# Kernel optimization log

Measured on AMD Instinct MI355X. Metric: run time of the kernel, lower is better.

Reference implementation:

```python
import math
import jax, jax.numpy as jnp
import numpy as np

BASE_MASK_PROB = 0.15
ENTROPY_TARGET = 0.7
MIN_ACTIVE = 1
EPS = 1e-8
NEG_LOG_EPS = -math.log(1e-8)

B, H, S = 4, 16, 1024


def setup_inputs() -> dict:
    key = jax.random.key(0)
    k1, k2 = jax.random.split(key)
    weights = jax.random.uniform(k1, (B, H, S, S), dtype=jnp.float32)
    # uniform noise replaces torch.bernoulli: mask = (noise < keep_prob)
    noise = jax.random.uniform(k2, (B, H, S, S), dtype=jnp.float32)
    return {"weights": weights, "noise": noise}


def _xlogy(x, y):
    # matches torch.xlogy: 0 * log(0) == 0
    return jnp.where(x == 0.0, 0.0, x * jnp.log(jnp.where(x == 0.0, 1.0, y)))


def reference(weights, noise):
    seq_len = weights.shape[-1]
    dtype = weights.dtype

    # normalize rows; degenerate (near-zero) rows become uniform
    weight_sums = jnp.sum(weights, axis=-1, keepdims=True)
    needs_norm = weight_sums < EPS
    safe_sums = jnp.where(needs_norm, 1.0, weight_sums)
    w = jnp.where(needs_norm, 1.0 / seq_len, weights / safe_sums)

    # fused entropy, clamped to -log(eps)
    entropy = jnp.minimum(-jnp.sum(_xlogy(w, w), axis=-1), NEG_LOG_EPS)

    max_entropy = math.log(float(seq_len))
    norm_entropy = jnp.clip(entropy / max_entropy, 0.0, 1.0)
    adaptive_prob = BASE_MASK_PROB * (1.0 - norm_entropy)
    keep_prob = 1.0 - adaptive_prob[..., None]          # [B,H,S,1]

    # bernoulli(keep_prob) via supplied uniform noise
    mask = (noise < keep_prob).astype(dtype)            # [B,H,S,S]

    # min_active fallback: rows with too few kept entries keep their top-k
    k = min(MIN_ACTIVE, seq_len)
    active_count = jnp.sum(mask, axis=-1)
    needs_more = active_count < k                        # [B,H,S]
    _, top_idx = jax.lax.top_k(w, k)                     # [B,H,S,k]
    min_mask = jnp.sum(jax.nn.one_hot(top_idx, seq_len, dtype=dtype), axis=-2)
    mask = jnp.where(needs_more[..., None], min_mask, mask)

    # mask and renormalize; fall back to unmasked weights if row sum ~ 0
    masked = w * mask
    msum = jnp.sum(masked, axis=-1, keepdims=True)
    valid = msum > EPS
    final_weights = jnp.where(valid, masked / jnp.where(valid, msum, 1.0), w)

    mask_rate = 1.0 - jnp.mean(mask, axis=-1)
    target_entropy = jnp.full_like(entropy, max_entropy * ENTROPY_TARGET)
    return final_weights, entropy, mask_rate, target_entropy
```

## Files before the change

### kernel.cpp

```cpp
#include <hip/hip_runtime.h>
#include <math.h>

namespace {
constexpr int kS = 1024;
constexpr float kEps = 1e-8f;
constexpr float kNegLogEps = 18.420680743952367f;
constexpr float kMaxEntropy = 6.9314718055994531f;
constexpr float kInvMaxEntropy = 1.0f / 6.9314718055994531f;
constexpr float kTargetEntropy = 4.8520302639196169f;
constexpr float kBaseMaskProb = 0.15f;
typedef float f32x4 __attribute__((ext_vector_type(4)));
}

__global__ __launch_bounds__(256, 8)
void curriculum_kernel(const float* __restrict__ weights,
                       const float* __restrict__ noise,
                       float* __restrict__ out_w,
                       float* __restrict__ out_ent,
                       float* __restrict__ out_mrate,
                       float* __restrict__ out_tent,
                       int nrows)
{
    const int lane = threadIdx.x & 63;
    const int wid  = threadIdx.x >> 6;
    const int row  = blockIdx.x * 4 + wid;
    if (row >= nrows) return;

    const long long base = (long long)row * kS;
    const float4* __restrict__ wsrc = reinterpret_cast<const float4*>(weights + base);
    const float4* __restrict__ nsrc = reinterpret_cast<const float4*>(noise + base);

    float4 a0 = wsrc[lane];
    float4 a1 = wsrc[lane + 64];
    float4 a2 = wsrc[lane + 128];
    float4 a3 = wsrc[lane + 192];
    float4 b0 = nsrc[lane];
    float4 b1 = nsrc[lane + 64];
    float4 b2 = nsrc[lane + 128];
    float4 b3 = nsrc[lane + 192];

    float w[16];
    w[0]=a0.x;  w[1]=a0.y;  w[2]=a0.z;  w[3]=a0.w;
    w[4]=a1.x;  w[5]=a1.y;  w[6]=a1.z;  w[7]=a1.w;
    w[8]=a2.x;  w[9]=a2.y;  w[10]=a2.z; w[11]=a2.w;
    w[12]=a3.x; w[13]=a3.y; w[14]=a3.z; w[15]=a3.w;

    float s = 0.0f, p = 0.0f;
    #pragma unroll
    for (int i = 0; i < 16; ++i) {
        s += w[i];
        p += w[i] * __logf(fmaxf(w[i], 1e-37f));
    }

    #pragma unroll
    for (int o = 1; o < 64; o <<= 1) {
        s += __shfl_xor(s, o, 64);
        p += __shfl_xor(p, o, 64);
    }

    if (s < kEps) {
        #pragma unroll
        for (int i = 0; i < 16; ++i) w[i] = 1.0f / (float)kS;
        s = 1.0f;
        p = -kMaxEntropy;
    }

    const float inv_s   = 1.0f / s;
    const float entropy = fminf(__logf(s) - p * inv_s, kNegLogEps);
    const float nent    = fminf(fmaxf(entropy * kInvMaxEntropy, 0.0f), 1.0f);
    const float keep    = 1.0f - kBaseMaskProb * (1.0f - nent);

    float nz[16];
    nz[0]=b0.x;  nz[1]=b0.y;  nz[2]=b0.z;  nz[3]=b0.w;
    nz[4]=b1.x;  nz[5]=b1.y;  nz[6]=b1.z;  nz[7]=b1.w;
    nz[8]=b2.x;  nz[9]=b2.y;  nz[10]=b2.z; nz[11]=b2.w;
    nz[12]=b3.x; nz[13]=b3.y; nz[14]=b3.z; nz[15]=b3.w;

    unsigned mask = 0u;
    float msum = 0.0f, cntf = 0.0f;
    #pragma unroll
    for (int i = 0; i < 16; ++i) {
        if (nz[i] < keep) { mask |= (1u << i); msum += w[i]; cntf += 1.0f; }
    }

    const unsigned long long anyk = __ballot(mask != 0u);

    #pragma unroll
    for (int o = 1; o < 64; o <<= 1) {
        cntf += __shfl_xor(cntf, o, 64);
        msum += __shfl_xor(msum, o, 64);
    }

    if (anyk == 0ull) {
        float mxv = w[0];
        int   mxi = lane * 4;
        #pragma unroll
        for (int i = 1; i < 16; ++i) {
            const int idx = ((i >> 2) << 8) + lane * 4 + (i & 3);
            if (w[i] > mxv) { mxv = w[i]; mxi = idx; }
        }
        #pragma unroll
        for (int o = 1; o < 64; o <<= 1) {
            const float ov = __shfl_xor(mxv, o, 64);
            const int   oi = __shfl_xor(mxi, o, 64);
            if (ov > mxv || (ov == mxv && oi < mxi)) { mxv = ov; mxi = oi; }
        }
        mask = (((mxi >> 2) & 63) == lane) ? (1u << (((mxi >> 8) << 2) | (mxi & 3))) : 0u;
        msum = mxv;
        cntf = 1.0f;
    }

    const bool  valid = msum > kEps * s;
    const float scale = valid ? 1.0f / msum : inv_s;

    f32x4 f0, f1, f2, f3;
    #pragma unroll
    for (int i = 0; i < 16; ++i) {
        const float v = (valid && !((mask >> i) & 1u)) ? 0.0f : w[i] * scale;
        f32x4* dstv = (i < 4) ? &f0 : (i < 8) ? &f1 : (i < 12) ? &f2 : &f3;
        (*dstv)[i & 3] = v;
    }

    f32x4* __restrict__ dst = reinterpret_cast<f32x4*>(out_w + base);
    __builtin_nontemporal_store(f0, dst + lane);
    __builtin_nontemporal_store(f1, dst + lane + 64);
    __builtin_nontemporal_store(f2, dst + lane + 128);
    __builtin_nontemporal_store(f3, dst + lane + 192);

    if (lane == 0) out_ent[row]   = entropy;
    if (lane == 1) out_mrate[row] = 1.0f - cntf * (1.0f / (float)kS);
    if (lane == 2) out_tent[row]  = kTargetEntropy;
}

extern "C" void kernel_launch(void* const* d_in, const int* in_sizes, int n_in,
                              void* d_out, int out_size, void* d_ws, size_t ws_size,
                              hipStream_t stream)
{
    (void)n_in; (void)d_ws; (void)ws_size; (void)out_size;

    const float* weights = (const float*)d_in[0];
    const float* noise   = (const float*)d_in[1];
    const long long total = (long long)in_sizes[0];
    const int nrows = (int)(total / kS);

    float* out_w     = (float*)d_out;
    float* out_ent   = out_w + total;
    float* out_mrate = out_ent + nrows;
    float* out_tent  = out_mrate + nrows;

    const int blocks = (nrows + 3) / 4;
    hipLaunchKernelGGL(curriculum_kernel, dim3(blocks), dim3(256), 0, stream,
                       weights, noise, out_w, out_ent, out_mrate, out_tent, nrows);
}
```

Measured before the change: 143.4 us.

## Process multiple rows per wave with register prefetch of next row

Each wave now handles eight rows in a grid-stride loop, loading the next row's weights and noise into registers while the current row is reduced and written. The aim is to overlap global load latency with compute and to cut the number of launched blocks. It doubles register use and lowers occupancy (launch bounds 4 instead of 8). With fewer blocks the GPU may also be less evenly filled.

```diff
diff --git a/kernel.cpp b/kernel.cpp
--- a/kernel.cpp
+++ b/kernel.cpp
@@ -9,36 +9,19 @@
 constexpr float kInvMaxEntropy = 1.0f / 6.9314718055994531f;
 constexpr float kTargetEntropy = 4.8520302639196169f;
 constexpr float kBaseMaskProb = 0.15f;
+constexpr int kRowsPerWave = 8;
 typedef float f32x4 __attribute__((ext_vector_type(4)));
 }
 
-__global__ __launch_bounds__(256, 8)
-void curriculum_kernel(const float* __restrict__ weights,
-                       const float* __restrict__ noise,
-                       float* __restrict__ out_w,
-                       float* __restrict__ out_ent,
-                       float* __restrict__ out_mrate,
-                       float* __restrict__ out_tent,
-                       int nrows)
+__device__ __forceinline__ void process_row(
+    f32x4 a0, f32x4 a1, f32x4 a2, f32x4 a3,
+    f32x4 b0, f32x4 b1, f32x4 b2, f32x4 b3,
+    int row, int lane,
+    float* __restrict__ out_w,
+    float* __restrict__ out_ent,
+    float* __restrict__ out_mrate,
+    float* __restrict__ out_tent)
 {
-    const int lane = threadIdx.x & 63;
-    const int wid  = threadIdx.x >> 6;
-    const int row  = blockIdx.x * 4 + wid;
-    if (row >= nrows) return;
-
-    const long long base = (long long)row * kS;
-    const float4* __restrict__ wsrc = reinterpret_cast<const float4*>(weights + base);
-    const float4* __restrict__ nsrc = reinterpret_cast<const float4*>(noise + base);
-
-    float4 a0 = wsrc[lane];
-    float4 a1 = wsrc[lane + 64];
-    float4 a2 = wsrc[lane + 128];
-    float4 a3 = wsrc[lane + 192];
-    float4 b0 = nsrc[lane];
-    float4 b1 = nsrc[lane + 64];
-    float4 b2 = nsrc[lane + 128];
-    float4 b3 = nsrc[lane + 192];
-
     float w[16];
     w[0]=a0.x;  w[1]=a0.y;  w[2]=a0.z;  w[3]=a0.w;
     w[4]=a1.x;  w[5]=a1.y;  w[6]=a1.z;  w[7]=a1.w;
@@ -51,7 +34,6 @@
         s += w[i];
         p += w[i] * __logf(fmaxf(w[i], 1e-37f));
     }
-
     #pragma unroll
     for (int o = 1; o < 64; o <<= 1) {
         s += __shfl_xor(s, o, 64);
@@ -121,7 +103,7 @@
         (*dstv)[i & 3] = v;
     }
 
-    f32x4* __restrict__ dst = reinterpret_cast<f32x4*>(out_w + base);
+    f32x4* __restrict__ dst = reinterpret_cast<f32x4*>(out_w + ((long long)row << 10));
     __builtin_nontemporal_store(f0, dst + lane);
     __builtin_nontemporal_store(f1, dst + lane + 64);
     __builtin_nontemporal_store(f2, dst + lane + 128);
@@ -130,6 +112,46 @@
     if (lane == 0) out_ent[row]   = entropy;
     if (lane == 1) out_mrate[row] = 1.0f - cntf * (1.0f / (float)kS);
     if (lane == 2) out_tent[row]  = kTargetEntropy;
+}
+
+__global__ __launch_bounds__(256, 4)
+void curriculum_kernel(const float* __restrict__ weights,
+                       const float* __restrict__ noise,
+                       float* __restrict__ out_w,
+                       float* __restrict__ out_ent,
+                       float* __restrict__ out_mrate,
+                       float* __restrict__ out_tent,
+                       int nrows, int wstride)
+{
+    const int lane = threadIdx.x & 63;
+    int row = (blockIdx.x << 2) | (threadIdx.x >> 6);
+    if (row >= nrows) return;
+
+    const f32x4* __restrict__ ws = reinterpret_cast<const f32x4*>(weights + ((long long)row << 10));
+    const f32x4* __restrict__ ns = reinterpret_cast<const f32x4*>(noise   + ((long long)row << 10));
+    f32x4 a0 = ws[lane], a1 = ws[lane+64], a2 = ws[lane+128], a3 = ws[lane+192];
+    f32x4 b0 = ns[lane], b1 = ns[lane+64], b2 = ns[lane+128], b3 = ns[lane+192];
+
+    for (int k = 0; k < kRowsPerWave; ++k) {
+        const int nrow = row + wstride;
+        const bool pf = (k + 1 < kRowsPerWave) && (nrow < nrows);
+
+        f32x4 na0, na1, na2, na3, nb0, nb1, nb2, nb3;
+        if (pf) {
+            const f32x4* nw = reinterpret_cast<const f32x4*>(weights + ((long long)nrow << 10));
+            const f32x4* nn = reinterpret_cast<const f32x4*>(noise   + ((long long)nrow << 10));
+            na0 = nw[lane]; na1 = nw[lane+64]; na2 = nw[lane+128]; na3 = nw[lane+192];
+            nb0 = nn[lane]; nb1 = nn[lane+64]; nb2 = nn[lane+128]; nb3 = nn[lane+192];
+        }
+
+        process_row(a0, a1, a2, a3, b0, b1, b2, b3, row, lane,
+                    out_w, out_ent, out_mrate, out_tent);
+
+        if (!pf) break;
+        row = nrow;
+        a0 = na0; a1 = na1; a2 = na2; a3 = na3;
+        b0 = nb0; b1 = nb1; b2 = nb2; b3 = nb3;
+    }
 }
 
 extern "C" void kernel_launch(void* const* d_in, const int* in_sizes, int n_in,
@@ -148,7 +170,11 @@
     float* out_mrate = out_ent + nrows;
     float* out_tent  = out_mrate + nrows;
 
-    const int blocks = (nrows + 3) / 4;
+    const int rows_per_block = 4 * kRowsPerWave;
+    const int blocks = (nrows + rows_per_block - 1) / rows_per_block;
+    const int wstride = blocks * 4;
+
     hipLaunchKernelGGL(curriculum_kernel, dim3(blocks), dim3(256), 0, stream,
-                       weights, noise, out_w, out_ent, out_mrate, out_tent, nrows);
+                       weights, noise, out_w, out_ent, out_mrate, out_tent,
+                       nrows, wstride);
 }
```

Result: slower. 150.0 us (+4.6%).
